# Kernel tuning notes

Hardware: AMD Instinct MI355X
Metric: run time of the kernel (lower is better)

Reference implementation:

```python
import jax, jax.numpy as jnp
import numpy as np

EPS = 1e-8


def setup_inputs() -> dict:
    key = jax.random.key(0)
    ks = jax.random.split(key, 8)
    B, N, D = 8, 1024, 256
    x = jax.random.normal(ks[0], (B, N, D), dtype=jnp.float32)
    y = jax.random.normal(ks[1], (B, N, D), dtype=jnp.float32)
    coords = jax.random.normal(ks[2], (N, N, 6), dtype=jnp.float32)
    # xavier-ish init for U, kaiming-ish for S1/S2
    U = jax.random.normal(ks[3], (D, D), dtype=jnp.float32) * (1.0 / np.sqrt(D))
    S1 = jax.random.normal(ks[4], (D, 1), dtype=jnp.float32)
    S2 = jax.random.normal(ks[5], (D, 1), dtype=jnp.float32)
    gating = jnp.asarray(1.0, dtype=jnp.float32)
    h_temp = jnp.asarray(0.1, dtype=jnp.float32)
    p_temp = jnp.asarray(1.0, dtype=jnp.float32)
    # trunc_normal_(a=0, b=1): std-normal truncated to [0, 1]
    pos_emb = jax.random.truncated_normal(ks[6], 0.0, 1.0, (N, 6, 1)).astype(jnp.float32)
    return {"x": x, "y": y, "coords": coords, "U": U, "S1": S1, "S2": S2,
            "gating": gating, "h_temp": h_temp, "p_temp": p_temp, "pos_emb": pos_emb}


def _spectral(x, U, S):
    # x @ U.T @ diag(|S|) @ U  ==  ((x @ U.T) * |S|) @ U
    s = jnp.abs(S[:, 0])
    return ((x @ U.T) * s) @ U


def reference(x, y, coords, U, S1, S2, gating, h_temp, p_temp, pos_emb):
    B, N, D = x.shape
    scale = D ** (-0.5)
    xs = jnp.stack([_spectral(x, U, S1), _spectral(x, U, S2)], axis=1)  # [B,2,N,D]
    # patch attention scores: [B,2,N,N]
    patch_score = jax.nn.softmax(jnp.einsum('bknd,bmd->bknm', xs, y) * scale, axis=-1)
    # positional scores, shared across batch and the 2 spectral branches: [N,N]
    pos_logits = -jnp.abs(p_temp) * jnp.einsum('nmc,ncq->nm', coords, pos_emb)
    pos_score = jax.nn.softmax(pos_logits, axis=-1)
    g = jax.nn.sigmoid(gating)
    attn = (1.0 - g) * patch_score + g * pos_score[None, None]  # [B,2,N,N]
    # entropy over key axis -> [B,N,2]
    entropy = jnp.sum(-attn * jnp.log(attn + EPS), axis=-1).transpose(0, 2, 1)
    hmap = 2.0 - 2.0 * jax.nn.sigmoid(h_temp * entropy)  # [B,N,2]
    fgbg = hmap[..., 0] >= hmap[..., 1]
    route = jax.lax.stop_gradient(
        jnp.stack([fgbg, ~fgbg], axis=-1).astype(hmap.dtype))  # [B,N,2]
    heat_map = jnp.sum(hmap * route, axis=-1, keepdims=True)  # [B,N,1]
    attn_sel = jnp.sum(attn * route.transpose(0, 2, 1)[..., None], axis=1)  # [B,N,N]
    out = attn_sel @ y  # [B,N,D]
    return (out, heat_map)
```

## Files before the change

### kernel.cpp

```cpp
#include <hip/hip_runtime.h>
#include <hip/hip_bf16.h>
#include <stdint.h>


#define NB 8
#define NN_ 1024
#define ND 256

typedef __bf16 bf16x8 __attribute__((ext_vector_type(8)));
typedef __bf16 bf16x4 __attribute__((ext_vector_type(4)));
typedef float f32x4 __attribute__((ext_vector_type(4)));

__device__ inline void gl_lds(const __bf16* g, __bf16* l) {
    auto gp = (const __attribute__((address_space(1))) uint32_t*)(uintptr_t)g;
    auto lp = (__attribute__((address_space(3))) uint32_t*)(uintptr_t)l;
    __builtin_amdgcn_global_load_lds(gp, lp, 16, 0, 0);
}

__device__ inline float wred_sum(float v) {
#pragma unroll
    for (int o = 32; o; o >>= 1) v += __shfl_xor(v, o, 64);
    return v;
}
__device__ inline float wred_max(float v) {
#pragma unroll
    for (int o = 32; o; o >>= 1) v = fmaxf(v, __shfl_xor(v, o, 64));
    return v;
}

__global__ __launch_bounds__(256) void prep_kernel(
    const float* __restrict__ coords, const float* __restrict__ pos_emb,
    const float* __restrict__ p_temp, const float* __restrict__ x,
    const float* __restrict__ y, const float* __restrict__ U,
    const float* __restrict__ S1, const float* __restrict__ S2,
    float* __restrict__ posS, __bf16* __restrict__ Xh, __bf16* __restrict__ Xl,
    __bf16* __restrict__ yt, __bf16* __restrict__ Yh, __bf16* __restrict__ Yl,
    __bf16* __restrict__ Mh, __bf16* __restrict__ Ml) {
    __shared__ char sm[9216 + 64];
    const int bid = blockIdx.x;
    const int tid = threadIdx.x;

    if (bid < 1024) {
        float* red = (float*)sm;
        const int n = bid;
        const float pt = -fabsf(p_temp[0]);
        float pe[6];
#pragma unroll
        for (int c = 0; c < 6; ++c) pe[c] = pos_emb[n * 6 + c];
        const float* cr = coords + (long)n * NN_ * 6;
        float l[4];
#pragma unroll
        for (int j = 0; j < 4; ++j) {
            const int m = j * 256 + tid;
            const float2* cp = (const float2*)(cr + (long)m * 6);
            float2 c0 = cp[0], c1 = cp[1], c2 = cp[2];
            l[j] = pt * (c0.x * pe[0] + c0.y * pe[1] + c1.x * pe[2] +
                         c1.y * pe[3] + c2.x * pe[4] + c2.y * pe[5]);
        }
        float mx = fmaxf(fmaxf(l[0], l[1]), fmaxf(l[2], l[3]));
        mx = wred_max(mx);
        __syncthreads();
        if ((tid & 63) == 0) red[tid >> 6] = mx;
        __syncthreads();
        mx = fmaxf(fmaxf(red[0], red[1]), fmaxf(red[2], red[3]));
        float e[4], s = 0.f;
#pragma unroll
        for (int j = 0; j < 4; ++j) { e[j] = __expf(l[j] - mx); s += e[j]; }
        s = wred_sum(s);
        __syncthreads();
        if ((tid & 63) == 0) red[4 + (tid >> 6)] = s;
        __syncthreads();
        s = red[4] + red[5] + red[6] + red[7];
        const float inv = 1.f / s;
#pragma unroll
        for (int j = 0; j < 4; ++j)
            posS[(long)n * NN_ + j * 256 + tid] = e[j] * inv;
    } else if (bid < 1536) {
        const int n4 = NB * NN_ * ND / 4;
        int i = (bid - 1024) * 256 + tid;
        for (; i < n4; i += 512 * 256) {
            float4 v = ((const float4*)x)[i];
            bf16x4 h, l;
            h[0] = (__bf16)v.x; l[0] = (__bf16)(v.x - (float)h[0]);
            h[1] = (__bf16)v.y; l[1] = (__bf16)(v.y - (float)h[1]);
            h[2] = (__bf16)v.z; l[2] = (__bf16)(v.z - (float)h[2]);
            h[3] = (__bf16)v.w; l[3] = (__bf16)(v.w - (float)h[3]);
            ((bf16x4*)Xh)[i] = h;
            ((bf16x4*)Xl)[i] = l;
        }
    } else if (bid < 2048) {
        __bf16 (*t)[72] = (__bf16(*)[72])sm;
        const int rem = bid - 1536;
        const int b = rem >> 6;
        const int m0 = (rem & 15) * 64, d0 = ((rem >> 4) & 3) * 64;
        const int c = tid & 15;
        const int r = tid >> 4;
#pragma unroll
        for (int p = 0; p < 4; ++p) {
            const int row = r + p * 16;
            const long gi = ((long)b * NN_ + m0 + row) * ND + d0 + c * 4;
            float4 v = *(const float4*)(y + gi);
            bf16x4 h, l;
            h[0] = (__bf16)v.x; l[0] = (__bf16)(v.x - (float)h[0]);
            h[1] = (__bf16)v.y; l[1] = (__bf16)(v.y - (float)h[1]);
            h[2] = (__bf16)v.z; l[2] = (__bf16)(v.z - (float)h[2]);
            h[3] = (__bf16)v.w; l[3] = (__bf16)(v.w - (float)h[3]);
            *(bf16x4*)(Yh + gi) = h;
            *(bf16x4*)(Yl + gi) = l;
            t[c * 4 + 0][row] = h[0]; t[c * 4 + 1][row] = h[1];
            t[c * 4 + 2][row] = h[2]; t[c * 4 + 3][row] = h[3];
        }
        __syncthreads();
#pragma unroll
        for (int p = 0; p < 4; ++p) {
            const int d = r + p * 16;
            bf16x4 o;
            o[0] = t[d][c * 4 + 0]; o[1] = t[d][c * 4 + 1];
            o[2] = t[d][c * 4 + 2]; o[3] = t[d][c * 4 + 3];
            *(bf16x4*)(yt + ((long)b * ND + d0 + d) * NN_ + m0 + c * 4) = o;
        }
    } else {
        const int n = bid - 2048, j = tid;
        float a1 = 0.f, a2 = 0.f;
        for (int c = 0; c < ND; ++c) {
            const float un = U[c * ND + n];
            const float uj = U[c * ND + j];
            a1 = fmaf(fabsf(S1[c]) * un, uj, a1);
            a2 = fmaf(fabsf(S2[c]) * un, uj, a2);
        }
        const __bf16 h1 = (__bf16)a1, h2 = (__bf16)a2;
        Mh[n * ND + j] = h1;           Ml[n * ND + j] = (__bf16)(a1 - (float)h1);
        Mh[65536 + n * ND + j] = h2;   Ml[65536 + n * ND + j] = (__bf16)(a2 - (float)h2);
    }
}

__global__ __launch_bounds__(256) void mgemm_xs(
    const __bf16* __restrict__ Ah, const __bf16* __restrict__ Al,
    const __bf16* __restrict__ Bh, const __bf16* __restrict__ Bl,
    __bf16* __restrict__ Ch, __bf16* __restrict__ Cl,
    int M, int N, int K, long sB1, long sC) {
    constexpr int BM = 128, BK = 32, BN = 64;
    __shared__ __bf16 As[2 * BM * BK];
    __shared__ __bf16 Bs[2 * BN * BK];

    const int z = blockIdx.z;
    Bh += (long)z * sB1; Bl += (long)z * sB1;

    const int tid = threadIdx.x;
    const int bm = blockIdx.y * BM, bn = blockIdx.x * BN;
    const int wave = tid >> 6, lane = tid & 63;
    const int wm = wave >> 1, wn = wave & 1;
    const int quad = lane >> 4, l16 = lane & 15;

    f32x4 acc[4][2];
#pragma unroll
    for (int i = 0; i < 4; ++i)
#pragma unroll
        for (int j = 0; j < 2; ++j) acc[i][j] = (f32x4){0.f, 0.f, 0.f, 0.f};

    const int srow = lane >> 2;
    const int slot = lane & 3;

    for (int k0 = 0; k0 < K; k0 += BK) {
        __syncthreads();
#pragma unroll
        for (int i = 0; i < 2; ++i) {
            const int r0 = wave * 32 + i * 16;
            const int row = r0 + srow;
            const int chunk = slot ^ ((row >> 1) & 3);
            const long g = (long)(bm + row) * K + k0 + chunk * 8;
            gl_lds(Ah + g, &As[r0 * 32]);
            gl_lds(Al + g, &As[BM * BK + r0 * 32]);
        }
        {
            const int r0 = wave * 16;
            const int row = r0 + srow;
            const int chunk = slot ^ ((row >> 1) & 3);
            const long g = (long)(bn + row) * K + k0 + chunk * 8;
            gl_lds(Bh + g, &Bs[r0 * 32]);
            gl_lds(Bl + g, &Bs[BN * BK + r0 * 32]);
        }
        __syncthreads();

        bf16x8 a_h[4], a_l[4], b_h[2], b_l[2];
#pragma unroll
        for (int mi = 0; mi < 4; ++mi) {
            const int row = wm * 64 + mi * 16 + l16;
            const int off = row * 32 + ((quad ^ ((row >> 1) & 3)) * 8);
            a_h[mi] = *(const bf16x8*)&As[off];
            a_l[mi] = *(const bf16x8*)&As[BM * BK + off];
        }
#pragma unroll
        for (int ni = 0; ni < 2; ++ni) {
            const int row = wn * 32 + ni * 16 + l16;
            const int off = row * 32 + ((quad ^ ((row >> 1) & 3)) * 8);
            b_h[ni] = *(const bf16x8*)&Bs[off];
            b_l[ni] = *(const bf16x8*)&Bs[BN * BK + off];
        }
#pragma unroll
        for (int mi = 0; mi < 4; ++mi)
#pragma unroll
            for (int ni = 0; ni < 2; ++ni) {
                acc[mi][ni] = __builtin_amdgcn_mfma_f32_16x16x32_bf16(
                    a_h[mi], b_h[ni], acc[mi][ni], 0, 0, 0);
                acc[mi][ni] = __builtin_amdgcn_mfma_f32_16x16x32_bf16(
                    a_h[mi], b_l[ni], acc[mi][ni], 0, 0, 0);
                acc[mi][ni] = __builtin_amdgcn_mfma_f32_16x16x32_bf16(
                    a_l[mi], b_h[ni], acc[mi][ni], 0, 0, 0);
            }
    }

    Ch += (long)z * sC; Cl += (long)z * sC;
#pragma unroll
    for (int mi = 0; mi < 4; ++mi) {
        const int row0 = bm + wm * 64 + mi * 16 + quad * 4;
#pragma unroll
        for (int ni = 0; ni < 2; ++ni) {
            const int col = bn + wn * 32 + ni * 16 + l16;
#pragma unroll
            for (int r = 0; r < 4; ++r) {
                const float v = acc[mi][ni][r];
                const long idx = (long)(row0 + r) * N + col;
                const __bf16 h = (__bf16)v;
                Ch[idx] = h;
                Cl[idx] = (__bf16)(v - (float)h);
            }
        }
    }
}

__global__ __launch_bounds__(256) void mgemm_sc(
    const __bf16* __restrict__ Ah, const __bf16* __restrict__ Al,
    const __bf16* __restrict__ Bh, const __bf16* __restrict__ Bl,
    float* __restrict__ C, int N, int K,
    long sA1, long sA2, long sB1, long sC, float alpha) {
    constexpr int BM = 128, BK = 32, BN = 128;
    __shared__ __bf16 As[2 * BM * BK];
    __shared__ __bf16 Bs[2 * BN * BK];

    const int z = blockIdx.z;
    const long aoff = (long)(z >> 1) * sA1 + (long)(z & 1) * sA2;
    const long boff = (long)(z >> 1) * sB1;
    Ah += aoff; Al += aoff;
    Bh += boff; Bl += boff;

    const int tid = threadIdx.x;
    const int bm = blockIdx.y * BM, bn = blockIdx.x * BN;
    const int wave = tid >> 6, lane = tid & 63;
    const int wm = wave >> 1, wn = wave & 1;
    const int quad = lane >> 4, l16 = lane & 15;

    f32x4 acc[4][4];
#pragma unroll
    for (int i = 0; i < 4; ++i)
#pragma unroll
        for (int j = 0; j < 4; ++j) acc[i][j] = (f32x4){0.f, 0.f, 0.f, 0.f};

    const int srow = lane >> 2;
    const int slot = lane & 3;

    for (int k0 = 0; k0 < K; k0 += BK) {
        __syncthreads();
#pragma unroll
        for (int i = 0; i < 2; ++i) {
            const int r0 = wave * 32 + i * 16;
            const int row = r0 + srow;
            const int chunk = slot ^ ((row >> 1) & 3);
            const long ga = (long)(bm + row) * K + k0 + chunk * 8;
            gl_lds(Ah + ga, &As[r0 * 32]);
            gl_lds(Al + ga, &As[BM * BK + r0 * 32]);
            const long gb = (long)(bn + row) * K + k0 + chunk * 8;
            gl_lds(Bh + gb, &Bs[r0 * 32]);
            gl_lds(Bl + gb, &Bs[BN * BK + r0 * 32]);
        }
        __syncthreads();

        bf16x8 a_h[4], a_l[4], b_h[4], b_l[4];
#pragma unroll
        for (int mi = 0; mi < 4; ++mi) {
            const int row = wm * 64 + mi * 16 + l16;
            const int off = row * 32 + ((quad ^ ((row >> 1) & 3)) * 8);
            a_h[mi] = *(const bf16x8*)&As[off];
            a_l[mi] = *(const bf16x8*)&As[BM * BK + off];
        }
#pragma unroll
        for (int ni = 0; ni < 4; ++ni) {
            const int row = wn * 64 + ni * 16 + l16;
            const int off = row * 32 + ((quad ^ ((row >> 1) & 3)) * 8);
            b_h[ni] = *(const bf16x8*)&Bs[off];
            b_l[ni] = *(const bf16x8*)&Bs[BN * BK + off];
        }
#pragma unroll
        for (int mi = 0; mi < 4; ++mi)
#pragma unroll
            for (int ni = 0; ni < 4; ++ni) {
                acc[mi][ni] = __builtin_amdgcn_mfma_f32_16x16x32_bf16(
                    a_h[mi], b_h[ni], acc[mi][ni], 0, 0, 0);
                acc[mi][ni] = __builtin_amdgcn_mfma_f32_16x16x32_bf16(
                    a_h[mi], b_l[ni], acc[mi][ni], 0, 0, 0);
                acc[mi][ni] = __builtin_amdgcn_mfma_f32_16x16x32_bf16(
                    a_l[mi], b_h[ni], acc[mi][ni], 0, 0, 0);
            }
    }

    C += (long)z * sC;
#pragma unroll
    for (int mi = 0; mi < 4; ++mi) {
        const int row0 = bm + wm * 64 + mi * 16 + quad * 4;
#pragma unroll
        for (int ni = 0; ni < 4; ++ni) {
            const int col = bn + wn * 64 + ni * 16 + l16;
#pragma unroll
            for (int r = 0; r < 4; ++r)
                C[(long)(row0 + r) * NN_ + col] = acc[mi][ni][r] * alpha;
        }
    }
}

__global__ __launch_bounds__(256, 8) void blendsm_kernel(
    const float* __restrict__ S, const float* __restrict__ pos,
    const float* __restrict__ gating, const float* __restrict__ h_temp,
    __bf16* __restrict__ P, float* __restrict__ heat) {
    const int b = blockIdx.x & 7;
    const int n = (blockIdx.x >> 3) * 4 + (threadIdx.x >> 6);
    const int lane = threadIdx.x & 63;

    const float g = 1.f / (1.f + __expf(-gating[0]));
    const float cg = 1.f - g;
    const float ht = h_temp[0];

    const float* r0p = S + ((long)(b * 2 + 0) * NN_ + n) * NN_;
    const float* r1p = S + ((long)(b * 2 + 1) * NN_ + n) * NN_;

    float4 a0[4], a1[4];
#pragma unroll
    for (int j = 0; j < 4; ++j) {
        a0[j] = *(const float4*)(r0p + j * 256 + lane * 4);
        a1[j] = *(const float4*)(r1p + j * 256 + lane * 4);
    }
    float m0 = -3.4e38f, m1 = -3.4e38f;
#pragma unroll
    for (int j = 0; j < 4; ++j) {
        m0 = fmaxf(m0, fmaxf(fmaxf(a0[j].x, a0[j].y), fmaxf(a0[j].z, a0[j].w)));
        m1 = fmaxf(m1, fmaxf(fmaxf(a1[j].x, a1[j].y), fmaxf(a1[j].z, a1[j].w)));
    }
    m0 = wred_max(m0); m1 = wred_max(m1);
    float s0 = 0.f, s1 = 0.f;
#pragma unroll
    for (int j = 0; j < 4; ++j) {
        a0[j].x = __expf(a0[j].x - m0); a0[j].y = __expf(a0[j].y - m0);
        a0[j].z = __expf(a0[j].z - m0); a0[j].w = __expf(a0[j].w - m0);
        s0 += a0[j].x + a0[j].y + a0[j].z + a0[j].w;
        a1[j].x = __expf(a1[j].x - m1); a1[j].y = __expf(a1[j].y - m1);
        a1[j].z = __expf(a1[j].z - m1); a1[j].w = __expf(a1[j].w - m1);
        s1 += a1[j].x + a1[j].y + a1[j].z + a1[j].w;
    }
    s0 = wred_sum(s0); s1 = wred_sum(s1);
    const float i0 = 1.f / s0, i1 = 1.f / s1;
    const float* pr = pos + (long)n * NN_;
    float e0 = 0.f, e1 = 0.f;
#pragma unroll
    for (int j = 0; j < 4; ++j) {
        const float4 pv = *(const float4*)(pr + j * 256 + lane * 4);
        a0[j].x = cg * a0[j].x * i0 + g * pv.x;
        a0[j].y = cg * a0[j].y * i0 + g * pv.y;
        a0[j].z = cg * a0[j].z * i0 + g * pv.z;
        a0[j].w = cg * a0[j].w * i0 + g * pv.w;
        a1[j].x = cg * a1[j].x * i1 + g * pv.x;
        a1[j].y = cg * a1[j].y * i1 + g * pv.y;
        a1[j].z = cg * a1[j].z * i1 + g * pv.z;
        a1[j].w = cg * a1[j].w * i1 + g * pv.w;
        e0 -= a0[j].x * __logf(a0[j].x + 1e-8f) + a0[j].y * __logf(a0[j].y + 1e-8f) +
              a0[j].z * __logf(a0[j].z + 1e-8f) + a0[j].w * __logf(a0[j].w + 1e-8f);
        e1 -= a1[j].x * __logf(a1[j].x + 1e-8f) + a1[j].y * __logf(a1[j].y + 1e-8f) +
              a1[j].z * __logf(a1[j].z + 1e-8f) + a1[j].w * __logf(a1[j].w + 1e-8f);
    }
    e0 = wred_sum(e0); e1 = wred_sum(e1);
    const float hm0 = 2.f - 2.f / (1.f + __expf(-ht * e0));
    const float hm1 = 2.f - 2.f / (1.f + __expf(-ht * e1));
    const bool fg = (hm0 >= hm1);
    if (lane == 0) heat[(long)b * NN_ + n] = fg ? hm0 : hm1;
    __bf16* prow = P + ((long)b * NN_ + n) * NN_;
#pragma unroll
    for (int j = 0; j < 4; ++j) {
        const float4 v = fg ? a0[j] : a1[j];
        bf16x4 o;
        o[0] = (__bf16)v.x; o[1] = (__bf16)v.y;
        o[2] = (__bf16)v.z; o[3] = (__bf16)v.w;
        *(bf16x4*)(prow + j * 256 + lane * 4) = o;
    }
}

__global__ __launch_bounds__(256) void pv_gemm(
    const __bf16* __restrict__ A, const __bf16* __restrict__ Bm,
    float* __restrict__ C) {
    constexpr int BM = 128, BK = 32, BN = 64;
    __shared__ __bf16 As[2][BM * BK];
    __shared__ __bf16 Bs[2][BN * BK];

    const int z = blockIdx.z;
    A  += (long)z * NN_ * NN_;
    Bm += (long)z * ND * NN_;
    C  += (long)z * NN_ * ND;

    const int tid = threadIdx.x;
    const int bm = blockIdx.y * BM, bn = blockIdx.x * BN;
    const int wave = tid >> 6, lane = tid & 63;
    const int wm = wave >> 1, wn = wave & 1;
    const int quad = lane >> 4, l16 = lane & 15;
    const int srow = lane >> 2, slot = lane & 3;

    f32x4 acc[4][2];
#pragma unroll
    for (int i = 0; i < 4; ++i)
#pragma unroll
        for (int j = 0; j < 2; ++j) acc[i][j] = (f32x4){0.f, 0.f, 0.f, 0.f};

    auto stage = [&](int sel, int k0) {
#pragma unroll
        for (int i = 0; i < 2; ++i) {
            const int r0 = wave * 32 + i * 16;
            const int row = r0 + srow;
            const int chunk = slot ^ ((row >> 1) & 3);
            gl_lds(A + (long)(bm + row) * NN_ + k0 + chunk * 8, &As[sel][r0 * 32]);
        }
        {
            const int r0 = wave * 16;
            const int row = r0 + srow;
            const int chunk = slot ^ ((row >> 1) & 3);
            gl_lds(Bm + (long)(bn + row) * NN_ + k0 + chunk * 8, &Bs[sel][r0 * 32]);
        }
    };

    stage(0, 0);
    __syncthreads();
    int cur = 0;
    for (int k0 = 0; k0 < NN_; k0 += BK) {
        if (k0 + BK < NN_) stage(cur ^ 1, k0 + BK);

        bf16x8 a[4], bb[2];
#pragma unroll
        for (int mi = 0; mi < 4; ++mi) {
            const int row = wm * 64 + mi * 16 + l16;
            const int off = row * 32 + ((quad ^ ((row >> 1) & 3)) * 8);
            a[mi] = *(const bf16x8*)&As[cur][off];
        }
#pragma unroll
        for (int ni = 0; ni < 2; ++ni) {
            const int row = wn * 32 + ni * 16 + l16;
            const int off = row * 32 + ((quad ^ ((row >> 1) & 3)) * 8);
            bb[ni] = *(const bf16x8*)&Bs[cur][off];
        }
#pragma unroll
        for (int mi = 0; mi < 4; ++mi)
#pragma unroll
            for (int ni = 0; ni < 2; ++ni)
                acc[mi][ni] = __builtin_amdgcn_mfma_f32_16x16x32_bf16(
                    a[mi], bb[ni], acc[mi][ni], 0, 0, 0);

        __syncthreads();
        cur ^= 1;
    }

#pragma unroll
    for (int mi = 0; mi < 4; ++mi) {
        const int row0 = bm + wm * 64 + mi * 16 + quad * 4;
#pragma unroll
        for (int ni = 0; ni < 2; ++ni) {
            const int col = bn + wn * 32 + ni * 16 + l16;
#pragma unroll
            for (int r = 0; r < 4; ++r)
                C[(long)(row0 + r) * ND + col] = acc[mi][ni][r];
        }
    }
}

extern "C" void kernel_launch(void* const* d_in, const int* in_sizes, int n_in,
                              void* d_out, int out_size, void* d_ws, size_t ws_size,
                              hipStream_t stream) {
    const float* x      = (const float*)d_in[0];
    const float* y      = (const float*)d_in[1];
    const float* coords = (const float*)d_in[2];
    const float* U      = (const float*)d_in[3];
    const float* S1p    = (const float*)d_in[4];
    const float* S2p    = (const float*)d_in[5];
    const float* gating = (const float*)d_in[6];
    const float* h_temp = (const float*)d_in[7];
    const float* p_temp = (const float*)d_in[8];
    const float* pos_emb= (const float*)d_in[9];

    float* out  = (float*)d_out;
    float* heat = out + (long)NB * NN_ * ND;

    char* ws = (char*)d_ws;
    const long MB = 1 << 20;
    float*  Sf  = (float*)(ws);
    float*  pos = (float*)(ws + 64 * MB);
    __bf16* Xh  = (__bf16*)(ws + 68 * MB);
    __bf16* Xl  = (__bf16*)(ws + 72 * MB);
    __bf16* XSh = (__bf16*)(ws + 76 * MB);
    __bf16* XSl = (__bf16*)(ws + 84 * MB);
    __bf16* yt  = (__bf16*)(ws + 92 * MB);
    __bf16* Yh  = (__bf16*)(ws + 96 * MB);
    __bf16* Yl  = (__bf16*)(ws + 100 * MB);
    __bf16* Mh  = (__bf16*)(ws + 104 * MB);
    __bf16* Ml  = Mh + 2 * 65536;
    __bf16* Pb  = (__bf16*)(ws + 76 * MB);

    const long ND2 = (long)NN_ * ND;
    const long BND = (long)NB * ND2;

    prep_kernel<<<dim3(2304), 256, 0, stream>>>(
        coords, pos_emb, p_temp, x, y, U, S1p, S2p,
        pos, Xh, Xl, yt, Yh, Yl, Mh, Ml);

    mgemm_xs<<<dim3(4, 64, 2), 256, 0, stream>>>(
        Xh, Xl, Mh, Ml, XSh, XSl, NB * NN_, ND, ND, 65536, BND);

    mgemm_sc<<<dim3(8, 8, NB * 2), 256, 0, stream>>>(
        XSh, XSl, Yh, Yl, Sf, NN_, ND,
        ND2, BND, ND2, (long)NN_ * NN_, 0.0625f);

    blendsm_kernel<<<dim3(2048), 256, 0, stream>>>(
        Sf, pos, gating, h_temp, Pb, heat);

    pv_gemm<<<dim3(4, 8, 8), 256, 0, stream>>>(Pb, yt, out);

    (void)in_sizes; (void)n_in; (void)out_size; (void)ws_size;
}
```

Before: 216.0 us.

## Double-buffer LDS tiles in score GEMM and use nontemporal stores/loads

The split-bf16 score GEMM now holds two LDS buffers and issues the next K-tile's global-to-LDS loads before computing on the current tile, with one barrier per iteration instead of two. This is meant to hide global load latency behind MFMA work. Score-matrix and output writes, and the score reads in the blend/softmax kernel, become nontemporal to reduce cache pollution from streaming data. LDS use per block doubles, which can lower occupancy. The prefetch is issued without an explicit wait before the end-of-iteration barrier, so whether the next tile has landed in LDS when it is read depends on how the compiler places the wait.

After: 210.2 us. 1.03x faster.

```diff
diff --git a/kernel.cpp b/kernel.cpp
--- a/kernel.cpp
+++ b/kernel.cpp
@@ -235,8 +235,8 @@
     float* __restrict__ C, int N, int K,
     long sA1, long sA2, long sB1, long sC, float alpha) {
     constexpr int BM = 128, BK = 32, BN = 128;
-    __shared__ __bf16 As[2 * BM * BK];
-    __shared__ __bf16 Bs[2 * BN * BK];
+    __shared__ __bf16 As[2][2 * BM * BK];
+    __shared__ __bf16 Bs[2][2 * BN * BK];
 
     const int z = blockIdx.z;
     const long aoff = (long)(z >> 1) * sA1 + (long)(z & 1) * sA2;
@@ -259,36 +259,41 @@
     const int srow = lane >> 2;
     const int slot = lane & 3;
 
-    for (int k0 = 0; k0 < K; k0 += BK) {
-        __syncthreads();
+    auto stage = [&](int sel, int k0) {
 #pragma unroll
         for (int i = 0; i < 2; ++i) {
             const int r0 = wave * 32 + i * 16;
             const int row = r0 + srow;
             const int chunk = slot ^ ((row >> 1) & 3);
             const long ga = (long)(bm + row) * K + k0 + chunk * 8;
-            gl_lds(Ah + ga, &As[r0 * 32]);
-            gl_lds(Al + ga, &As[BM * BK + r0 * 32]);
+            gl_lds(Ah + ga, &As[sel][r0 * 32]);
+            gl_lds(Al + ga, &As[sel][BM * BK + r0 * 32]);
             const long gb = (long)(bn + row) * K + k0 + chunk * 8;
-            gl_lds(Bh + gb, &Bs[r0 * 32]);
-            gl_lds(Bl + gb, &Bs[BN * BK + r0 * 32]);
-        }
-        __syncthreads();
+            gl_lds(Bh + gb, &Bs[sel][r0 * 32]);
+            gl_lds(Bl + gb, &Bs[sel][BN * BK + r0 * 32]);
+        }
+    };
+
+    stage(0, 0);
+    __syncthreads();
+    int cur = 0;
+    for (int k0 = 0; k0 < K; k0 += BK) {
+        if (k0 + BK < K) stage(cur ^ 1, k0 + BK);
 
         bf16x8 a_h[4], a_l[4], b_h[4], b_l[4];
 #pragma unroll
         for (int mi = 0; mi < 4; ++mi) {
             const int row = wm * 64 + mi * 16 + l16;
             const int off = row * 32 + ((quad ^ ((row >> 1) & 3)) * 8);
-            a_h[mi] = *(const bf16x8*)&As[off];
-            a_l[mi] = *(const bf16x8*)&As[BM * BK + off];
+            a_h[mi] = *(const bf16x8*)&As[cur][off];
+            a_l[mi] = *(const bf16x8*)&As[cur][BM * BK + off];
         }
 #pragma unroll
         for (int ni = 0; ni < 4; ++ni) {
             const int row = wn * 64 + ni * 16 + l16;
             const int off = row * 32 + ((quad ^ ((row >> 1) & 3)) * 8);
-            b_h[ni] = *(const bf16x8*)&Bs[off];
-            b_l[ni] = *(const bf16x8*)&Bs[BN * BK + off];
+            b_h[ni] = *(const bf16x8*)&Bs[cur][off];
+            b_l[ni] = *(const bf16x8*)&Bs[cur][BN * BK + off];
         }
 #pragma unroll
         for (int mi = 0; mi < 4; ++mi)
@@ -301,6 +306,9 @@
                 acc[mi][ni] = __builtin_amdgcn_mfma_f32_16x16x32_bf16(
                     a_l[mi], b_h[ni], acc[mi][ni], 0, 0, 0);
             }
+
+        __syncthreads();
+        cur ^= 1;
     }
 
     C += (long)z * sC;
@@ -312,7 +320,8 @@
             const int col = bn + wn * 64 + ni * 16 + l16;
 #pragma unroll
             for (int r = 0; r < 4; ++r)
-                C[(long)(row0 + r) * NN_ + col] = acc[mi][ni][r] * alpha;
+                __builtin_nontemporal_store(acc[mi][ni][r] * alpha,
+                                            &C[(long)(row0 + r) * NN_ + col]);
         }
     }
 }
@@ -332,28 +341,28 @@
     const float* r0p = S + ((long)(b * 2 + 0) * NN_ + n) * NN_;
     const float* r1p = S + ((long)(b * 2 + 1) * NN_ + n) * NN_;
 
-    float4 a0[4], a1[4];
+    f32x4 a0[4], a1[4];
 #pragma unroll
     for (int j = 0; j < 4; ++j) {
-        a0[j] = *(const float4*)(r0p + j * 256 + lane * 4);
-        a1[j] = *(const float4*)(r1p + j * 256 + lane * 4);
+        a0[j] = __builtin_nontemporal_load((const f32x4*)(r0p + j * 256 + lane * 4));
+        a1[j] = __builtin_nontemporal_load((const f32x4*)(r1p + j * 256 + lane * 4));
     }
     float m0 = -3.4e38f, m1 = -3.4e38f;
 #pragma unroll
     for (int j = 0; j < 4; ++j) {
-        m0 = fmaxf(m0, fmaxf(fmaxf(a0[j].x, a0[j].y), fmaxf(a0[j].z, a0[j].w)));
-        m1 = fmaxf(m1, fmaxf(fmaxf(a1[j].x, a1[j].y), fmaxf(a1[j].z, a1[j].w)));
+        m0 = fmaxf(m0, fmaxf(fmaxf(a0[j][0], a0[j][1]), fmaxf(a0[j][2], a0[j][3])));
+        m1 = fmaxf(m1, fmaxf(fmaxf(a1[j][0], a1[j][1]), fmaxf(a1[j][2], a1[j][3])));
     }
     m0 = wred_max(m0); m1 = wred_max(m1);
     float s0 = 0.f, s1 = 0.f;
 #pragma unroll
     for (int j = 0; j < 4; ++j) {
-        a0[j].x = __expf(a0[j].x - m0); a0[j].y = __expf(a0[j].y - m0);
-        a0[j].z = __expf(a0[j].z - m0); a0[j].w = __expf(a0[j].w - m0);
-        s0 += a0[j].x + a0[j].y + a0[j].z + a0[j].w;
-        a1[j].x = __expf(a1[j].x - m1); a1[j].y = __expf(a1[j].y - m1);
-        a1[j].z = __expf(a1[j].z - m1); a1[j].w = __expf(a1[j].w - m1);
-        s1 += a1[j].x + a1[j].y + a1[j].z + a1[j].w;
+        a0[j][0] = __expf(a0[j][0] - m0); a0[j][1] = __expf(a0[j][1] - m0);
+        a0[j][2] = __expf(a0[j][2] - m0); a0[j][3] = __expf(a0[j][3] - m0);
+        s0 += a0[j][0] + a0[j][1] + a0[j][2] + a0[j][3];
+        a1[j][0] = __expf(a1[j][0] - m1); a1[j][1] = __expf(a1[j][1] - m1);
+        a1[j][2] = __expf(a1[j][2] - m1); a1[j][3] = __expf(a1[j][3] - m1);
+        s1 += a1[j][0] + a1[j][1] + a1[j][2] + a1[j][3];
     }
     s0 = wred_sum(s0); s1 = wred_sum(s1);
     const float i0 = 1.f / s0, i1 = 1.f / s1;
@@ -361,19 +370,19 @@
     float e0 = 0.f, e1 = 0.f;
 #pragma unroll
     for (int j = 0; j < 4; ++j) {
-        const float4 pv = *(const float4*)(pr + j * 256 + lane * 4);
-        a0[j].x = cg * a0[j].x * i0 + g * pv.x;
-        a0[j].y = cg * a0[j].y * i0 + g * pv.y;
-        a0[j].z = cg * a0[j].z * i0 + g * pv.z;
-        a0[j].w = cg * a0[j].w * i0 + g * pv.w;
-        a1[j].x = cg * a1[j].x * i1 + g * pv.x;
-        a1[j].y = cg * a1[j].y * i1 + g * pv.y;
-        a1[j].z = cg * a1[j].z * i1 + g * pv.z;
-        a1[j].w = cg * a1[j].w * i1 + g * pv.w;
-        e0 -= a0[j].x * __logf(a0[j].x + 1e-8f) + a0[j].y * __logf(a0[j].y + 1e-8f) +
-              a0[j].z * __logf(a0[j].z + 1e-8f) + a0[j].w * __logf(a0[j].w + 1e-8f);
-        e1 -= a1[j].x * __logf(a1[j].x + 1e-8f) + a1[j].y * __logf(a1[j].y + 1e-8f) +
-              a1[j].z * __logf(a1[j].z + 1e-8f) + a1[j].w * __logf(a1[j].w + 1e-8f);
+        const f32x4 pv = *(const f32x4*)(pr + j * 256 + lane * 4);
+        a0[j][0] = cg * a0[j][0] * i0 + g * pv[0];
+        a0[j][1] = cg * a0[j][1] * i0 + g * pv[1];
+        a0[j][2] = cg * a0[j][2] * i0 + g * pv[2];
+        a0[j][3] = cg * a0[j][3] * i0 + g * pv[3];
+        a1[j][0] = cg * a1[j][0] * i1 + g * pv[0];
+        a1[j][1] = cg * a1[j][1] * i1 + g * pv[1];
+        a1[j][2] = cg * a1[j][2] * i1 + g * pv[2];
+        a1[j][3] = cg * a1[j][3] * i1 + g * pv[3];
+        e0 -= a0[j][0] * __logf(a0[j][0] + 1e-8f) + a0[j][1] * __logf(a0[j][1] + 1e-8f) +
+              a0[j][2] * __logf(a0[j][2] + 1e-8f) + a0[j][3] * __logf(a0[j][3] + 1e-8f);
+        e1 -= a1[j][0] * __logf(a1[j][0] + 1e-8f) + a1[j][1] * __logf(a1[j][1] + 1e-8f) +
+              a1[j][2] * __logf(a1[j][2] + 1e-8f) + a1[j][3] * __logf(a1[j][3] + 1e-8f);
     }
     e0 = wred_sum(e0); e1 = wred_sum(e1);
     const float hm0 = 2.f - 2.f / (1.f + __expf(-ht * e0));
@@ -383,10 +392,10 @@
     __bf16* prow = P + ((long)b * NN_ + n) * NN_;
 #pragma unroll
     for (int j = 0; j < 4; ++j) {
-        const float4 v = fg ? a0[j] : a1[j];
+        const f32x4 v = fg ? a0[j] : a1[j];
         bf16x4 o;
-        o[0] = (__bf16)v.x; o[1] = (__bf16)v.y;
-        o[2] = (__bf16)v.z; o[3] = (__bf16)v.w;
+        o[0] = (__bf16)v[0]; o[1] = (__bf16)v[1];
+        o[2] = (__bf16)v[2]; o[3] = (__bf16)v[3];
         *(bf16x4*)(prow + j * 256 + lane * 4) = o;
     }
 }
@@ -470,7 +479,8 @@
             const int col = bn + wn * 32 + ni * 16 + l16;
 #pragma unroll
             for (int r = 0; r < 4; ++r)
-                C[(long)(row0 + r) * ND + col] = acc[mi][ni][r];
+                __builtin_nontemporal_store(acc[mi][ni][r],
+                                            &C[(long)(row0 + r) * ND + col]);
         }
     }
 }
```

## Fuse score GEMM with softmax, positional blend and entropy routing

Applied to the files above, without the earlier changes.

Replaces the separate score GEMM, which wrote a 64 MB fp32 score tensor, and the blend/softmax kernel with one fused kernel. Each block computes full 1024-wide score rows for 16 query rows and both spectral branches in registers. It then performs softmax, the positional blend, entropy and routing in-register, using cross-wave LDS reductions. This removes the large score-matrix round trip through global memory. In exchange, the Y operand is read straight from global memory without LDS staging, register pressure is high (128 accumulators per thread), and only 512 blocks are launched, so occupancy is low.

New measurement: 217.9 us. No clear change (+0.8%).

```diff
diff --git a/kernel.cpp b/kernel.cpp
--- a/kernel.cpp
+++ b/kernel.cpp
@@ -229,165 +229,218 @@
     }
 }
 
-__global__ __launch_bounds__(256) void mgemm_sc(
-    const __bf16* __restrict__ Ah, const __bf16* __restrict__ Al,
-    const __bf16* __restrict__ Bh, const __bf16* __restrict__ Bl,
-    float* __restrict__ C, int N, int K,
-    long sA1, long sA2, long sB1, long sC, float alpha) {
-    constexpr int BM = 128, BK = 32, BN = 128;
-    __shared__ __bf16 As[2 * BM * BK];
-    __shared__ __bf16 Bs[2 * BN * BK];
-
-    const int z = blockIdx.z;
-    const long aoff = (long)(z >> 1) * sA1 + (long)(z & 1) * sA2;
-    const long boff = (long)(z >> 1) * sB1;
-    Ah += aoff; Al += aoff;
-    Bh += boff; Bl += boff;
-
+__global__ __launch_bounds__(256, 2) void scblend_kernel(
+    const __bf16* __restrict__ XSh, const __bf16* __restrict__ XSl,
+    const __bf16* __restrict__ Yh, const __bf16* __restrict__ Yl,
+    const float* __restrict__ pos, const float* __restrict__ gating,
+    const float* __restrict__ h_temp, __bf16* __restrict__ P,
+    float* __restrict__ heat) {
+    __shared__ __bf16 Asm[2][2][16][256];
+    __shared__ float red_max[4][2][16];
+    __shared__ float red_sum[4][2][16];
+    __shared__ float red_ent[4][2][16];
+
+    const int b  = blockIdx.x & 7;
+    const int n0 = (blockIdx.x >> 3) * 16;
     const int tid = threadIdx.x;
-    const int bm = blockIdx.y * BM, bn = blockIdx.x * BN;
     const int wave = tid >> 6, lane = tid & 63;
-    const int wm = wave >> 1, wn = wave & 1;
     const int quad = lane >> 4, l16 = lane & 15;
 
-    f32x4 acc[4][4];
-#pragma unroll
-    for (int i = 0; i < 4; ++i)
-#pragma unroll
-        for (int j = 0; j < 4; ++j) acc[i][j] = (f32x4){0.f, 0.f, 0.f, 0.f};
-
-    const int srow = lane >> 2;
-    const int slot = lane & 3;
-
-    for (int k0 = 0; k0 < K; k0 += BK) {
-        __syncthreads();
-#pragma unroll
-        for (int i = 0; i < 2; ++i) {
-            const int r0 = wave * 32 + i * 16;
-            const int row = r0 + srow;
-            const int chunk = slot ^ ((row >> 1) & 3);
-            const long ga = (long)(bm + row) * K + k0 + chunk * 8;
-            gl_lds(Ah + ga, &As[r0 * 32]);
-            gl_lds(Al + ga, &As[BM * BK + r0 * 32]);
-            const long gb = (long)(bn + row) * K + k0 + chunk * 8;
-            gl_lds(Bh + gb, &Bs[r0 * 32]);
-            gl_lds(Bl + gb, &Bs[BN * BK + r0 * 32]);
-        }
-        __syncthreads();
-
-        bf16x8 a_h[4], a_l[4], b_h[4], b_l[4];
-#pragma unroll
-        for (int mi = 0; mi < 4; ++mi) {
-            const int row = wm * 64 + mi * 16 + l16;
-            const int off = row * 32 + ((quad ^ ((row >> 1) & 3)) * 8);
-            a_h[mi] = *(const bf16x8*)&As[off];
-            a_l[mi] = *(const bf16x8*)&As[BM * BK + off];
-        }
-#pragma unroll
-        for (int ni = 0; ni < 4; ++ni) {
-            const int row = wn * 64 + ni * 16 + l16;
-            const int off = row * 32 + ((quad ^ ((row >> 1) & 3)) * 8);
-            b_h[ni] = *(const bf16x8*)&Bs[off];
-            b_l[ni] = *(const bf16x8*)&Bs[BN * BK + off];
-        }
-#pragma unroll
-        for (int mi = 0; mi < 4; ++mi)
-#pragma unroll
-            for (int ni = 0; ni < 4; ++ni) {
-                acc[mi][ni] = __builtin_amdgcn_mfma_f32_16x16x32_bf16(
-                    a_h[mi], b_h[ni], acc[mi][ni], 0, 0, 0);
-                acc[mi][ni] = __builtin_amdgcn_mfma_f32_16x16x32_bf16(
-                    a_h[mi], b_l[ni], acc[mi][ni], 0, 0, 0);
-                acc[mi][ni] = __builtin_amdgcn_mfma_f32_16x16x32_bf16(
-                    a_l[mi], b_h[ni], acc[mi][ni], 0, 0, 0);
-            }
-    }
-
-    C += (long)z * sC;
-#pragma unroll
-    for (int mi = 0; mi < 4; ++mi) {
-        const int row0 = bm + wm * 64 + mi * 16 + quad * 4;
-#pragma unroll
-        for (int ni = 0; ni < 4; ++ni) {
-            const int col = bn + wn * 64 + ni * 16 + l16;
-#pragma unroll
-            for (int r = 0; r < 4; ++r)
-                C[(long)(row0 + r) * NN_ + col] = acc[mi][ni][r] * alpha;
-        }
-    }
-}
-
-__global__ __launch_bounds__(256, 8) void blendsm_kernel(
-    const float* __restrict__ S, const float* __restrict__ pos,
-    const float* __restrict__ gating, const float* __restrict__ h_temp,
-    __bf16* __restrict__ P, float* __restrict__ heat) {
-    const int b = blockIdx.x & 7;
-    const int n = (blockIdx.x >> 3) * 4 + (threadIdx.x >> 6);
-    const int lane = threadIdx.x & 63;
+    const long BND = (long)NB * NN_ * ND;
+    const long bA  = (long)b * NN_ * ND;
+
+    {
+        __bf16* lbase = &Asm[0][0][0][0];
+#pragma unroll
+        for (int i = 0; i < 8; ++i) {
+            const int c   = i * 256 + tid;
+            const int ch  = c & 31;
+            const int row = (c >> 5) & 15;
+            const int hl  = (c >> 9) & 1;
+            const int mi  = c >> 10;
+            const int chg = ch ^ (row & 7);
+            const __bf16* src = (hl ? XSl : XSh) + (long)mi * BND + bA +
+                                (long)(n0 + row) * ND + chg * 8;
+            gl_lds(src, lbase + (i * 256 + wave * 64) * 8);
+        }
+    }
+    __syncthreads();
+
+    f32x4 acc[2][16];
+#pragma unroll
+    for (int mi = 0; mi < 2; ++mi)
+#pragma unroll
+        for (int n = 0; n < 16; ++n) acc[mi][n] = (f32x4){0.f, 0.f, 0.f, 0.f};
+
+    const int colbase = wave * 256;
+#pragma unroll
+    for (int ks = 0; ks < 8; ++ks) {
+        bf16x8 af[2][2];
+#pragma unroll
+        for (int mi = 0; mi < 2; ++mi)
+#pragma unroll
+            for (int hl = 0; hl < 2; ++hl) {
+                const int ch = (ks * 4 + quad) ^ (l16 & 7);
+                af[mi][hl] = *(const bf16x8*)&Asm[mi][hl][l16][ch * 8];
+            }
+#pragma unroll
+        for (int n = 0; n < 16; ++n) {
+            const long ky = (bA + (long)(colbase + n * 16 + l16) * ND) +
+                            ks * 32 + quad * 8;
+            bf16x8 bh = *(const bf16x8*)(Yh + ky);
+            bf16x8 bl = *(const bf16x8*)(Yl + ky);
+#pragma unroll
+            for (int mi = 0; mi < 2; ++mi) {
+                acc[mi][n] = __builtin_amdgcn_mfma_f32_16x16x32_bf16(
+                    af[mi][0], bh, acc[mi][n], 0, 0, 0);
+                acc[mi][n] = __builtin_amdgcn_mfma_f32_16x16x32_bf16(
+                    af[mi][0], bl, acc[mi][n], 0, 0, 0);
+                acc[mi][n] = __builtin_amdgcn_mfma_f32_16x16x32_bf16(
+                    af[mi][1], bh, acc[mi][n], 0, 0, 0);
+            }
+        }
+    }
+
+    const float alpha = 0.0625f;
+    float mrow[2][4];
+#pragma unroll
+    for (int mi = 0; mi < 2; ++mi)
+#pragma unroll
+        for (int r = 0; r < 4; ++r) mrow[mi][r] = -3.4e38f;
+#pragma unroll
+    for (int mi = 0; mi < 2; ++mi)
+#pragma unroll
+        for (int n = 0; n < 16; ++n)
+#pragma unroll
+            for (int r = 0; r < 4; ++r) {
+                acc[mi][n][r] *= alpha;
+                mrow[mi][r] = fmaxf(mrow[mi][r], acc[mi][n][r]);
+            }
+#pragma unroll
+    for (int o = 1; o < 16; o <<= 1)
+#pragma unroll
+        for (int mi = 0; mi < 2; ++mi)
+#pragma unroll
+            for (int r = 0; r < 4; ++r)
+                mrow[mi][r] = fmaxf(mrow[mi][r], __shfl_xor(mrow[mi][r], o, 64));
+    if (l16 == 0) {
+#pragma unroll
+        for (int mi = 0; mi < 2; ++mi)
+#pragma unroll
+            for (int r = 0; r < 4; ++r)
+                red_max[wave][mi][quad * 4 + r] = mrow[mi][r];
+    }
+    __syncthreads();
+#pragma unroll
+    for (int mi = 0; mi < 2; ++mi)
+#pragma unroll
+        for (int r = 0; r < 4; ++r) {
+            float m = red_max[0][mi][quad * 4 + r];
+            m = fmaxf(m, red_max[1][mi][quad * 4 + r]);
+            m = fmaxf(m, red_max[2][mi][quad * 4 + r]);
+            m = fmaxf(m, red_max[3][mi][quad * 4 + r]);
+            mrow[mi][r] = m;
+        }
+
+    float srow[2][4];
+#pragma unroll
+    for (int mi = 0; mi < 2; ++mi)
+#pragma unroll
+        for (int r = 0; r < 4; ++r) srow[mi][r] = 0.f;
+#pragma unroll
+    for (int mi = 0; mi < 2; ++mi)
+#pragma unroll
+        for (int n = 0; n < 16; ++n)
+#pragma unroll
+            for (int r = 0; r < 4; ++r) {
+                const float e = __expf(acc[mi][n][r] - mrow[mi][r]);
+                acc[mi][n][r] = e;
+                srow[mi][r] += e;
+            }
+#pragma unroll
+    for (int o = 1; o < 16; o <<= 1)
+#pragma unroll
+        for (int mi = 0; mi < 2; ++mi)
+#pragma unroll
+            for (int r = 0; r < 4; ++r)
+                srow[mi][r] += __shfl_xor(srow[mi][r], o, 64);
+    if (l16 == 0) {
+#pragma unroll
+        for (int mi = 0; mi < 2; ++mi)
+#pragma unroll
+            for (int r = 0; r < 4; ++r)
+                red_sum[wave][mi][quad * 4 + r] = srow[mi][r];
+    }
+    __syncthreads();
+    float irow[2][4];
+#pragma unroll
+    for (int mi = 0; mi < 2; ++mi)
+#pragma unroll
+        for (int r = 0; r < 4; ++r) {
+            const float s = red_sum[0][mi][quad * 4 + r] +
+                            red_sum[1][mi][quad * 4 + r] +
+                            red_sum[2][mi][quad * 4 + r] +
+                            red_sum[3][mi][quad * 4 + r];
+            irow[mi][r] = 1.f / s;
+        }
 
     const float g = 1.f / (1.f + __expf(-gating[0]));
     const float cg = 1.f - g;
     const float ht = h_temp[0];
-
-    const float* r0p = S + ((long)(b * 2 + 0) * NN_ + n) * NN_;
-    const float* r1p = S + ((long)(b * 2 + 1) * NN_ + n) * NN_;
-
-    float4 a0[4], a1[4];
-#pragma unroll
-    for (int j = 0; j < 4; ++j) {
-        a0[j] = *(const float4*)(r0p + j * 256 + lane * 4);
-        a1[j] = *(const float4*)(r1p + j * 256 + lane * 4);
-    }
-    float m0 = -3.4e38f, m1 = -3.4e38f;
-#pragma unroll
-    for (int j = 0; j < 4; ++j) {
-        m0 = fmaxf(m0, fmaxf(fmaxf(a0[j].x, a0[j].y), fmaxf(a0[j].z, a0[j].w)));
-        m1 = fmaxf(m1, fmaxf(fmaxf(a1[j].x, a1[j].y), fmaxf(a1[j].z, a1[j].w)));
-    }
-    m0 = wred_max(m0); m1 = wred_max(m1);
-    float s0 = 0.f, s1 = 0.f;
-#pragma unroll
-    for (int j = 0; j < 4; ++j) {
-        a0[j].x = __expf(a0[j].x - m0); a0[j].y = __expf(a0[j].y - m0);
-        a0[j].z = __expf(a0[j].z - m0); a0[j].w = __expf(a0[j].w - m0);
-        s0 += a0[j].x + a0[j].y + a0[j].z + a0[j].w;
-        a1[j].x = __expf(a1[j].x - m1); a1[j].y = __expf(a1[j].y - m1);
-        a1[j].z = __expf(a1[j].z - m1); a1[j].w = __expf(a1[j].w - m1);
-        s1 += a1[j].x + a1[j].y + a1[j].z + a1[j].w;
-    }
-    s0 = wred_sum(s0); s1 = wred_sum(s1);
-    const float i0 = 1.f / s0, i1 = 1.f / s1;
-    const float* pr = pos + (long)n * NN_;
-    float e0 = 0.f, e1 = 0.f;
-#pragma unroll
-    for (int j = 0; j < 4; ++j) {
-        const float4 pv = *(const float4*)(pr + j * 256 + lane * 4);
-        a0[j].x = cg * a0[j].x * i0 + g * pv.x;
-        a0[j].y = cg * a0[j].y * i0 + g * pv.y;
-        a0[j].z = cg * a0[j].z * i0 + g * pv.z;
-        a0[j].w = cg * a0[j].w * i0 + g * pv.w;
-        a1[j].x = cg * a1[j].x * i1 + g * pv.x;
-        a1[j].y = cg * a1[j].y * i1 + g * pv.y;
-        a1[j].z = cg * a1[j].z * i1 + g * pv.z;
-        a1[j].w = cg * a1[j].w * i1 + g * pv.w;
-        e0 -= a0[j].x * __logf(a0[j].x + 1e-8f) + a0[j].y * __logf(a0[j].y + 1e-8f) +
-              a0[j].z * __logf(a0[j].z + 1e-8f) + a0[j].w * __logf(a0[j].w + 1e-8f);
-        e1 -= a1[j].x * __logf(a1[j].x + 1e-8f) + a1[j].y * __logf(a1[j].y + 1e-8f) +
-              a1[j].z * __logf(a1[j].z + 1e-8f) + a1[j].w * __logf(a1[j].w + 1e-8f);
-    }
-    e0 = wred_sum(e0); e1 = wred_sum(e1);
-    const float hm0 = 2.f - 2.f / (1.f + __expf(-ht * e0));
-    const float hm1 = 2.f - 2.f / (1.f + __expf(-ht * e1));
-    const bool fg = (hm0 >= hm1);
-    if (lane == 0) heat[(long)b * NN_ + n] = fg ? hm0 : hm1;
-    __bf16* prow = P + ((long)b * NN_ + n) * NN_;
-#pragma unroll
-    for (int j = 0; j < 4; ++j) {
-        const float4 v = fg ? a0[j] : a1[j];
-        bf16x4 o;
-        o[0] = (__bf16)v.x; o[1] = (__bf16)v.y;
-        o[2] = (__bf16)v.z; o[3] = (__bf16)v.w;
-        *(bf16x4*)(prow + j * 256 + lane * 4) = o;
+    float erow[2][4];
+#pragma unroll
+    for (int mi = 0; mi < 2; ++mi)
+#pragma unroll
+        for (int r = 0; r < 4; ++r) erow[mi][r] = 0.f;
+#pragma unroll
+    for (int n = 0; n < 16; ++n) {
+        const int col = colbase + n * 16 + l16;
+        float pv[4];
+#pragma unroll
+        for (int r = 0; r < 4; ++r)
+            pv[r] = pos[(long)(n0 + quad * 4 + r) * NN_ + col];
+#pragma unroll
+        for (int mi = 0; mi < 2; ++mi)
+#pragma unroll
+            for (int r = 0; r < 4; ++r) {
+                const float p = cg * acc[mi][n][r] * irow[mi][r] + g * pv[r];
+                acc[mi][n][r] = p;
+                erow[mi][r] -= p * __logf(p + 1e-8f);
+            }
+    }
+#pragma unroll
+    for (int o = 1; o < 16; o <<= 1)
+#pragma unroll
+        for (int mi = 0; mi < 2; ++mi)
+#pragma unroll
+            for (int r = 0; r < 4; ++r)
+                erow[mi][r] += __shfl_xor(erow[mi][r], o, 64);
+    if (l16 == 0) {
+#pragma unroll
+        for (int mi = 0; mi < 2; ++mi)
+#pragma unroll
+            for (int r = 0; r < 4; ++r)
+                red_ent[wave][mi][quad * 4 + r] = erow[mi][r];
+    }
+    __syncthreads();
+
+#pragma unroll
+    for (int r = 0; r < 4; ++r) {
+        const float e0 = red_ent[0][0][quad * 4 + r] + red_ent[1][0][quad * 4 + r] +
+                         red_ent[2][0][quad * 4 + r] + red_ent[3][0][quad * 4 + r];
+        const float e1 = red_ent[0][1][quad * 4 + r] + red_ent[1][1][quad * 4 + r] +
+                         red_ent[2][1][quad * 4 + r] + red_ent[3][1][quad * 4 + r];
+        const float hm0 = 2.f - 2.f / (1.f + __expf(-ht * e0));
+        const float hm1 = 2.f - 2.f / (1.f + __expf(-ht * e1));
+        const bool fg = (hm0 >= hm1);
+        if (wave == 0 && l16 == 0)
+            heat[(long)b * NN_ + n0 + quad * 4 + r] = fg ? hm0 : hm1;
+        __bf16* prow = P + ((long)b * NN_ + n0 + quad * 4 + r) * NN_;
+#pragma unroll
+        for (int n = 0; n < 16; ++n) {
+            const float p = fg ? acc[0][n][r] : acc[1][n][r];
+            prow[colbase + n * 16 + l16] = (__bf16)p;
+        }
     }
 }
 
@@ -494,7 +547,7 @@
 
     char* ws = (char*)d_ws;
     const long MB = 1 << 20;
-    float*  Sf  = (float*)(ws);
+    __bf16* Pb  = (__bf16*)(ws);
     float*  pos = (float*)(ws + 64 * MB);
     __bf16* Xh  = (__bf16*)(ws + 68 * MB);
     __bf16* Xl  = (__bf16*)(ws + 72 * MB);
@@ -505,10 +558,8 @@
     __bf16* Yl  = (__bf16*)(ws + 100 * MB);
     __bf16* Mh  = (__bf16*)(ws + 104 * MB);
     __bf16* Ml  = Mh + 2 * 65536;
-    __bf16* Pb  = (__bf16*)(ws + 76 * MB);
-
-    const long ND2 = (long)NN_ * ND;
-    const long BND = (long)NB * ND2;
+
+    const long BND = (long)NB * NN_ * ND;
 
     prep_kernel<<<dim3(2304), 256, 0, stream>>>(
         coords, pos_emb, p_temp, x, y, U, S1p, S2p,
@@ -517,12 +568,8 @@
     mgemm_xs<<<dim3(4, 64, 2), 256, 0, stream>>>(
         Xh, Xl, Mh, Ml, XSh, XSl, NB * NN_, ND, ND, 65536, BND);
 
-    mgemm_sc<<<dim3(8, 8, NB * 2), 256, 0, stream>>>(
-        XSh, XSl, Yh, Yl, Sf, NN_, ND,
-        ND2, BND, ND2, (long)NN_ * NN_, 0.0625f);
-
-    blendsm_kernel<<<dim3(2048), 256, 0, stream>>>(
-        Sf, pos, gating, h_temp, Pb, heat);
+    scblend_kernel<<<dim3(512), 256, 0, stream>>>(
+        XSh, XSl, Yh, Yl, pos, gating, h_temp, Pb, heat);
 
     pv_gemm<<<dim3(4, 8, 8), 256, 0, stream>>>(Pb, yt, out);
 
```
